# Kernel tuning notes

Measured on AMD Instinct MI355X. Metric: run time of the kernel, lower is better.

Reference implementation:

```python
import jax, jax.numpy as jnp
import numpy as np

D_MODEL = 1024
N_HEADS = 16
SEQ = 512  # == max_seq_len; rel-pos bias requires n_token == max_seq_len


def setup_inputs() -> dict:
    key = jax.random.key(0)
    ks = jax.random.split(key, 12)
    B = 16
    x = jax.random.normal(ks[0], (B, SEQ, D_MODEL), dtype=jnp.float32)
    c = jax.random.normal(ks[1], (B, SEQ, 8), dtype=jnp.float32)  # unused by forward
    s = 1.0 / np.sqrt(D_MODEL)
    Wq = jax.random.normal(ks[2], (D_MODEL, D_MODEL), dtype=jnp.float32) * s
    bq = jnp.zeros((D_MODEL,), dtype=jnp.float32)
    Wk = jax.random.normal(ks[3], (D_MODEL, D_MODEL), dtype=jnp.float32) * s
    bk = jnp.zeros((D_MODEL,), dtype=jnp.float32)
    Wv = jax.random.normal(ks[4], (D_MODEL, D_MODEL), dtype=jnp.float32) * s
    bv = jnp.zeros((D_MODEL,), dtype=jnp.float32)
    Wo = jax.random.normal(ks[5], (D_MODEL, D_MODEL), dtype=jnp.float32) * s
    bo = jnp.zeros((D_MODEL,), dtype=jnp.float32)
    # trunc_normal_(std=0.02) approximated by normal*0.02 (values stay small)
    rel_table = jax.random.normal(ks[6], (2 * SEQ - 1, N_HEADS), dtype=jnp.float32) * 0.02
    return {"x": x, "c": c, "Wq": Wq, "bq": bq, "Wk": Wk, "bk": bk,
            "Wv": Wv, "bv": bv, "Wo": Wo, "bo": bo, "rel_table": rel_table}


def reference(x, c, Wq, bq, Wk, bk, Wv, bv, Wo, bo, rel_table):
    # x: [B, S, D]; c is unused in the original forward
    B, S, D = x.shape
    H = N_HEADS
    dk = D // H
    scale = 1.0 / np.sqrt(dk)

    q = (x @ Wq + bq).reshape(B, S, H, dk)
    k = (x @ Wk + bk).reshape(B, S, H, dk)
    v = (x @ Wv + bv).reshape(B, S, H, dk)

    # scores: [B, H, S, S]
    scores = jnp.einsum('bihd,bjhd->bhij', q, k) * scale

    # relative position bias: index[i,j] = i + (S-1-j), values in [0, 2S-2]
    rel_index = jnp.arange(S)[:, None] + jnp.arange(S - 1, -1, -1)[None, :]  # [S,S]
    bias = rel_table[rel_index]            # [S, S, H]
    scores = scores + jnp.transpose(bias, (2, 0, 1))[None]  # [1,H,S,S]

    # causal_mask=False: original adds False * -1e9 == 0, so no mask term
    probs = jax.nn.softmax(scores, axis=-1)

    out = jnp.einsum('bhij,bjhd->bihd', probs, v).reshape(B, S, D)
    return out @ Wo + bo
```

## Files before the change

kernel.cpp:

```cpp
#include <hip/hip_runtime.h>
#include <hip/hip_bf16.h>
#include <stdint.h>

#define D_MODEL 1024
#define NH 16
#define SEQ 512
#define DK 64
#define BATCH 16
#define M_TOT (BATCH*SEQ)

typedef unsigned short u16;
typedef unsigned int u32;
typedef __attribute__((ext_vector_type(8))) __bf16 bf16x8;
typedef __attribute__((ext_vector_type(4))) u16 ushort4v;
typedef __attribute__((ext_vector_type(4))) float f32x4;

static __device__ __forceinline__ u16 f2bf(float f) {
    union { float f; u32 i; } c; c.f = f;
    return (u16)((c.i + 0x8000u) >> 16);
}
static __device__ __forceinline__ void async_copy16(const void* g, void* l) {
    __builtin_amdgcn_global_load_lds(
        (const __attribute__((address_space(1))) u32*)g,
        (__attribute__((address_space(3))) u32*)l, 16, 0, 0);
}

__global__ __launch_bounds__(256) void convert_f32_bf16(const float* __restrict__ in,
                                                        u16* __restrict__ out) {
    const int i = (blockIdx.x * 256 + threadIdx.x) * 4;
    float4 v = *(const float4*)&in[i];
    ushort4v o;
    o[0] = f2bf(v.x); o[1] = f2bf(v.y); o[2] = f2bf(v.z); o[3] = f2bf(v.w);
    *(ushort4v*)&out[i] = o;
}

__global__ __launch_bounds__(256) void transpose_w3(const float* __restrict__ W0,
                                                    const float* __restrict__ W1,
                                                    const float* __restrict__ W2,
                                                    u16* __restrict__ Wt) {
    __shared__ u16 tile[64][65];
    const int z = blockIdx.z;
    const float* W = (z == 0) ? W0 : (z == 1) ? W1 : W2;
    const int n0 = blockIdx.x * 64, k0 = blockIdx.y * 64;
    const int t = threadIdx.x;
    #pragma unroll
    for (int p = 0; p < 16; ++p) {
        int idx = p * 256 + t;
        int r = idx >> 6, c = idx & 63;
        tile[r][c] = f2bf(W[(size_t)(k0 + r) * D_MODEL + (n0 + c)]);
    }
    __syncthreads();
    #pragma unroll
    for (int p = 0; p < 16; ++p) {
        int idx = p * 256 + t;
        int r = idx >> 6, c = idx & 63;
        Wt[((size_t)z * D_MODEL + n0 + r) * D_MODEL + (k0 + c)] = tile[c][r];
    }
}

__global__ __launch_bounds__(256) void gemm_bt(const u16* __restrict__ A,
                                               const u16* __restrict__ Bt,
                                               const float* __restrict__ b0,
                                               const float* __restrict__ b1,
                                               const float* __restrict__ b2,
                                               void* __restrict__ o0,
                                               void* __restrict__ o1,
                                               void* __restrict__ o2,
                                               int qkv) {
    __shared__ __attribute__((aligned(16))) u16 smem[16896];
    u16* Asm = smem;
    u16* Bsm = smem + 8192;
    const int t = threadIdx.x;
    const int m0 = blockIdx.y * 128, n0 = blockIdx.x * 128;
    const int lane = t & 63, w = t >> 6;
    const int lm = lane & 15, quad = lane >> 4;
    const int wm = w >> 1, wn = w & 1;

    f32x4 acc[4][4];
    #pragma unroll
    for (int i = 0; i < 4; ++i)
        #pragma unroll
        for (int j = 0; j < 4; ++j) acc[i][j] = (f32x4){0.f, 0.f, 0.f, 0.f};

    for (int kt = 0; kt < D_MODEL / 64; ++kt) {
        const int k0 = kt * 64;
        __syncthreads();
        #pragma unroll
        for (int i = 0; i < 4; ++i) {
            int chunk = i * 256 + t;
            int row = chunk >> 3, c = chunk & 7;
            int cs = c ^ (row & 7);
            async_copy16(A + (size_t)(m0 + row) * D_MODEL + k0 + cs * 8, &Asm[chunk * 8]);
        }
        #pragma unroll
        for (int i = 0; i < 4; ++i) {
            int chunk = i * 256 + t;
            int row = chunk >> 3, c = chunk & 7;
            int cs = c ^ (row & 7);
            async_copy16(Bt + (size_t)(n0 + row) * D_MODEL + k0 + cs * 8, &Bsm[chunk * 8]);
        }
        __syncthreads();
        #pragma unroll
        for (int ks = 0; ks < 64; ks += 32) {
            const int cbase = ks >> 3;
            bf16x8 af[4], bfv[4];
            #pragma unroll
            for (int im = 0; im < 4; ++im) {
                const int row = wm * 64 + im * 16 + lm;
                const int c = (cbase + quad) ^ (row & 7);
                af[im] = *(const bf16x8*)&Asm[row * 64 + c * 8];
            }
            #pragma unroll
            for (int in = 0; in < 4; ++in) {
                const int row = wn * 64 + in * 16 + lm;
                const int c = (cbase + quad) ^ (row & 7);
                bfv[in] = *(const bf16x8*)&Bsm[row * 64 + c * 8];
            }
            #pragma unroll
            for (int im = 0; im < 4; ++im)
                #pragma unroll
                for (int in = 0; in < 4; ++in)
                    acc[im][in] = __builtin_amdgcn_mfma_f32_16x16x32_bf16(
                        af[im], bfv[in], acc[im][in], 0, 0, 0);
        }
    }

    __syncthreads();
    if (qkv) {
        const int sel = n0 >> 10;
        if (sel == 2) {
            #pragma unroll
            for (int in = 0; in < 4; ++in) {
                const int nn = (n0 & 1023) + wn * 64 + in * 16 + lm;
                const float bv = b2[nn];
                const int h = nn >> 6, d = nn & 63;
                #pragma unroll
                for (int im = 0; im < 4; ++im) {
                    const int mb = m0 + wm * 64 + im * 16 + quad * 4;
                    const int b = mb >> 9, s = mb & 511;
                    ushort4v pk;
                    #pragma unroll
                    for (int r = 0; r < 4; ++r) pk[r] = f2bf(acc[im][in][r] + bv);
                    *(ushort4v*)&((u16*)o2)[((size_t)(b * NH + h) * DK + d) * SEQ + s] = pk;
                }
            }
        } else {
            u16* dst = sel ? (u16*)o1 : (u16*)o0;
            const float* bb = sel ? b1 : b0;
            u16 (*Cs)[132] = (u16(*)[132])smem;
            #pragma unroll
            for (int in = 0; in < 4; ++in) {
                const int nl = wn * 64 + in * 16 + lm;
                const float bv = bb[(n0 & 1023) + nl];
                #pragma unroll
                for (int im = 0; im < 4; ++im)
                    #pragma unroll
                    for (int r = 0; r < 4; ++r)
                        Cs[wm * 64 + im * 16 + quad * 4 + r][nl] =
                            f2bf(acc[im][in][r] + bv);
            }
            __syncthreads();
            const int rr = t >> 1, hh = t & 1;
            const int m = m0 + rr;
            const int b = m >> 9, s = m & 511;
            const int h = ((n0 & 1023) >> 6) + hh;
            u16* dp = &dst[((size_t)(b * NH + h) * SEQ + s) * DK];
            #pragma unroll
            for (int c = 0; c < 8; ++c)
                *(uint4*)&dp[c * 8] = *(const uint4*)&Cs[rr][hh * 64 + c * 8];
        }
    } else {
        float (*Cs)[132] = (float(*)[132])smem;
        #pragma unroll
        for (int ph = 0; ph < 2; ++ph) {
            if (wm == ph) {
                #pragma unroll
                for (int in = 0; in < 4; ++in) {
                    const int nl = wn * 64 + in * 16 + lm;
                    const float bv = b0[n0 + nl];
                    #pragma unroll
                    for (int im = 0; im < 4; ++im)
                        #pragma unroll
                        for (int r = 0; r < 4; ++r)
                            Cs[im * 16 + quad * 4 + r][nl] = acc[im][in][r] + bv;
                }
            }
            __syncthreads();
            const int rr = t >> 2, qq = t & 3;
            float* dp = &((float*)o0)[(size_t)(m0 + ph * 64 + rr) * D_MODEL + n0 + qq * 32];
            #pragma unroll
            for (int c = 0; c < 8; ++c)
                *(uint4*)&dp[c * 4] = *(const uint4*)&Cs[rr][qq * 32 + c * 4];
            __syncthreads();
        }
    }
}

__global__ __launch_bounds__(256) void attn_flash(const u16* __restrict__ qg,
                                                  const u16* __restrict__ kg,
                                                  const u16* __restrict__ vTg,
                                                  const float* __restrict__ rel,
                                                  u16* __restrict__ aout) {
    __shared__ __attribute__((aligned(16))) u16 qt[64][72];
    __shared__ __attribute__((aligned(16))) u16 kt[64][72];
    __shared__ __attribute__((aligned(16))) u16 vt[64][72];
    __shared__ __attribute__((aligned(16))) u16 Pl[4][16][72];
    __shared__ float biasb[576];

    const int t = threadIdx.x;
    const int lane = t & 63, w = t >> 6;
    const int lm = lane & 15, quad = lane >> 4;
    const int F = blockIdx.x;
    const int xcd = F & 7, qti = (F >> 3) & 7, grp = F >> 6;
    const int p = grp * 8 + xcd;
    const int h = p & 15, b = p >> 4;
    const int q0 = qti * 64;
    const size_t bh = (size_t)(b * NH + h);
    const u16* qb = qg + bh * SEQ * DK;
    const u16* kb = kg + bh * SEQ * DK;
    const u16* vb = vTg + bh * DK * SEQ;

    const int srow = t >> 3, scol = (t & 7) * 8;

    #pragma unroll
    for (int i = 0; i < 2; ++i)
        *(uint4*)&qt[i * 32 + srow][scol] = *(const uint4*)&qb[(q0 + i * 32 + srow) * DK + scol];
    for (int u = t; u < 575; u += 256) biasb[u] = rel[(q0 + u) * NH + h];

    uint4 kr[2], vr[2];
    kr[0] = *(const uint4*)&kb[srow * DK + scol];
    kr[1] = *(const uint4*)&kb[(32 + srow) * DK + scol];
    vr[0] = *(const uint4*)&vb[srow * SEQ + scol];
    vr[1] = *(const uint4*)&vb[(32 + srow) * SEQ + scol];

    float lsum[4] = {0.f, 0.f, 0.f, 0.f};
    f32x4 o[4];
    #pragma unroll
    for (int sd = 0; sd < 4; ++sd) o[sd] = (f32x4){0.f, 0.f, 0.f, 0.f};

    const float scale = 0.125f;

    for (int jt = 0; jt < 8; ++jt) {
        __syncthreads();
        *(uint4*)&kt[srow][scol] = kr[0];
        *(uint4*)&kt[32 + srow][scol] = kr[1];
        *(uint4*)&vt[srow][scol] = vr[0];
        *(uint4*)&vt[32 + srow][scol] = vr[1];
        __syncthreads();
        if (jt < 7) {
            const int j1 = (jt + 1) * 64;
            kr[0] = *(const uint4*)&kb[(j1 + srow) * DK + scol];
            kr[1] = *(const uint4*)&kb[(j1 + 32 + srow) * DK + scol];
            vr[0] = *(const uint4*)&vb[srow * SEQ + j1 + scol];
            vr[1] = *(const uint4*)&vb[(32 + srow) * SEQ + j1 + scol];
        }
        const int j0 = jt * 64;

        bf16x8 aq0 = *(const bf16x8*)&qt[w * 16 + lm][quad * 8];
        bf16x8 aq1 = *(const bf16x8*)&qt[w * 16 + lm][32 + quad * 8];
        #pragma unroll
        for (int js = 0; js < 4; ++js) {
            bf16x8 bk0 = *(const bf16x8*)&kt[js * 16 + lm][quad * 8];
            bf16x8 bk1 = *(const bf16x8*)&kt[js * 16 + lm][32 + quad * 8];
            f32x4 c = (f32x4){0.f, 0.f, 0.f, 0.f};
            c = __builtin_amdgcn_mfma_f32_16x16x32_bf16(aq0, bk0, c, 0, 0, 0);
            c = __builtin_amdgcn_mfma_f32_16x16x32_bf16(aq1, bk1, c, 0, 0, 0);
            const int jg = j0 + js * 16 + lm;
            #pragma unroll
            for (int r = 0; r < 4; ++r) {
                const int rl = w * 16 + quad * 4 + r;
                float e = __expf(c[r] * scale + biasb[rl + 511 - jg]);
                lsum[r] += e;
                Pl[w][quad * 4 + r][js * 16 + lm] = f2bf(e);
            }
        }

        bf16x8 ap0 = *(const bf16x8*)&Pl[w][lm][quad * 8];
        bf16x8 ap1 = *(const bf16x8*)&Pl[w][lm][32 + quad * 8];
        #pragma unroll
        for (int sd = 0; sd < 4; ++sd) {
            bf16x8 bv0 = *(const bf16x8*)&vt[sd * 16 + lm][quad * 8];
            bf16x8 bv1 = *(const bf16x8*)&vt[sd * 16 + lm][32 + quad * 8];
            o[sd] = __builtin_amdgcn_mfma_f32_16x16x32_bf16(ap0, bv0, o[sd], 0, 0, 0);
            o[sd] = __builtin_amdgcn_mfma_f32_16x16x32_bf16(ap1, bv1, o[sd], 0, 0, 0);
        }
    }

    #pragma unroll
    for (int r = 0; r < 4; ++r) {
        float s = lsum[r];
        s += __shfl_xor(s, 1, 64);
        s += __shfl_xor(s, 2, 64);
        s += __shfl_xor(s, 4, 64);
        s += __shfl_xor(s, 8, 64);
        const float rinv = 1.0f / s;
        const int srow2 = q0 + w * 16 + quad * 4 + r;
        #pragma unroll
        for (int sd = 0; sd < 4; ++sd)
            aout[(size_t)(b * SEQ + srow2) * D_MODEL + h * DK + sd * 16 + lm] =
                f2bf(o[sd][r] * rinv);
    }
}

extern "C" void kernel_launch(void* const* d_in, const int* in_sizes, int n_in,
                              void* d_out, int out_size, void* d_ws, size_t ws_size,
                              hipStream_t stream) {
    const float* x   = (const float*)d_in[0];
    const float* Wq  = (const float*)d_in[2];
    const float* bq  = (const float*)d_in[3];
    const float* Wk  = (const float*)d_in[4];
    const float* bk  = (const float*)d_in[5];
    const float* Wv  = (const float*)d_in[6];
    const float* bv  = (const float*)d_in[7];
    const float* Wo  = (const float*)d_in[8];
    const float* bo  = (const float*)d_in[9];
    const float* rel = (const float*)d_in[10];
    float* out = (float*)d_out;

    u16* ws = (u16*)d_ws;
    const size_t WSZ = (size_t)D_MODEL * D_MODEL;
    const size_t TSZ = (size_t)M_TOT * D_MODEL;
    u16* Wt3 = ws;
    u16* xbf = Wt3 + 3 * WSZ;
    u16* qws = xbf + TSZ;
    u16* kws = qws + TSZ;
    u16* vws = kws + TSZ;
    u16* aws = xbf;

    dim3 tb(256);
    convert_f32_bf16<<<dim3(M_TOT * D_MODEL / 1024), tb, 0, stream>>>(x, xbf);
    transpose_w3<<<dim3(16, 16, 3), tb, 0, stream>>>(Wq, Wk, Wv, Wt3);
    gemm_bt<<<dim3(24, 64), tb, 0, stream>>>(xbf, Wt3, bq, bk, bv, qws, kws, vws, 1);
    attn_flash<<<dim3(2048), tb, 0, stream>>>(qws, kws, vws, rel, aws);
    transpose_w3<<<dim3(16, 16, 1), tb, 0, stream>>>(Wo, Wo, Wo, Wt3);
    gemm_bt<<<dim3(8, 64), tb, 0, stream>>>(aws, Wt3, bo, nullptr, nullptr,
                                            (void*)out, nullptr, nullptr, 0);
}
```

Baseline: 301.2 us.

## Double-buffer K/V tiles with async LDS copies and coalesce attention output via head-major layout

Measured after the change: 264.5 us. 12.2% less time.

```diff
diff --git a/kernel.cpp b/kernel.cpp
--- a/kernel.cpp
+++ b/kernel.cpp
@@ -90,7 +90,15 @@
             int chunk = i * 256 + t;
             int row = chunk >> 3, c = chunk & 7;
             int cs = c ^ (row & 7);
-            async_copy16(A + (size_t)(m0 + row) * D_MODEL + k0 + cs * 8, &Asm[chunk * 8]);
+            const u16* src;
+            if (qkv) {
+                src = A + (size_t)(m0 + row) * D_MODEL + k0 + cs * 8;
+            } else {
+                const int m = m0 + row, g = kt * 8 + cs;
+                const int b = m >> 9, s = m & 511, h = g >> 3;
+                src = A + ((size_t)(b * NH + h) * SEQ + s) * DK + (g & 7) * 8;
+            }
+            async_copy16(src, &Asm[chunk * 8]);
         }
         #pragma unroll
         for (int i = 0; i < 4; ++i) {
@@ -201,9 +209,9 @@
                                                   const u16* __restrict__ vTg,
                                                   const float* __restrict__ rel,
                                                   u16* __restrict__ aout) {
-    __shared__ __attribute__((aligned(16))) u16 qt[64][72];
-    __shared__ __attribute__((aligned(16))) u16 kt[64][72];
-    __shared__ __attribute__((aligned(16))) u16 vt[64][72];
+    __shared__ __attribute__((aligned(16))) u16 qt[64 * 64];
+    __shared__ __attribute__((aligned(16))) u16 kt[2][64 * 64];
+    __shared__ __attribute__((aligned(16))) u16 vt[2][64 * 64];
     __shared__ __attribute__((aligned(16))) u16 Pl[4][16][72];
     __shared__ float biasb[576];
 
@@ -220,18 +228,21 @@
     const u16* kb = kg + bh * SEQ * DK;
     const u16* vb = vTg + bh * DK * SEQ;
 
-    const int srow = t >> 3, scol = (t & 7) * 8;
-
-    #pragma unroll
-    for (int i = 0; i < 2; ++i)
-        *(uint4*)&qt[i * 32 + srow][scol] = *(const uint4*)&qb[(q0 + i * 32 + srow) * DK + scol];
+    #pragma unroll
+    for (int i = 0; i < 2; ++i) {
+        const int chunk = i * 256 + t, row = chunk >> 3, c = chunk & 7;
+        const int cs = c ^ (row & 7);
+        *(uint4*)&qt[chunk * 8] = *(const uint4*)&qb[(q0 + row) * DK + cs * 8];
+    }
     for (int u = t; u < 575; u += 256) biasb[u] = rel[(q0 + u) * NH + h];
 
-    uint4 kr[2], vr[2];
-    kr[0] = *(const uint4*)&kb[srow * DK + scol];
-    kr[1] = *(const uint4*)&kb[(32 + srow) * DK + scol];
-    vr[0] = *(const uint4*)&vb[srow * SEQ + scol];
-    vr[1] = *(const uint4*)&vb[(32 + srow) * SEQ + scol];
+    #pragma unroll
+    for (int i = 0; i < 2; ++i) {
+        const int chunk = i * 256 + t, row = chunk >> 3, c = chunk & 7;
+        const int cs = c ^ (row & 7);
+        async_copy16(kb + row * DK + cs * 8, &kt[0][chunk * 8]);
+        async_copy16(vb + row * SEQ + cs * 8, &vt[0][chunk * 8]);
+    }
 
     float lsum[4] = {0.f, 0.f, 0.f, 0.f};
     f32x4 o[4];
@@ -242,26 +253,27 @@
 
     for (int jt = 0; jt < 8; ++jt) {
         __syncthreads();
-        *(uint4*)&kt[srow][scol] = kr[0];
-        *(uint4*)&kt[32 + srow][scol] = kr[1];
-        *(uint4*)&vt[srow][scol] = vr[0];
-        *(uint4*)&vt[32 + srow][scol] = vr[1];
-        __syncthreads();
+        const int cur = jt & 1, nxt = cur ^ 1;
         if (jt < 7) {
             const int j1 = (jt + 1) * 64;
-            kr[0] = *(const uint4*)&kb[(j1 + srow) * DK + scol];
-            kr[1] = *(const uint4*)&kb[(j1 + 32 + srow) * DK + scol];
-            vr[0] = *(const uint4*)&vb[srow * SEQ + j1 + scol];
-            vr[1] = *(const uint4*)&vb[(32 + srow) * SEQ + j1 + scol];
+            #pragma unroll
+            for (int i = 0; i < 2; ++i) {
+                const int chunk = i * 256 + t, row = chunk >> 3, c = chunk & 7;
+                const int cs = c ^ (row & 7);
+                async_copy16(kb + (j1 + row) * DK + cs * 8, &kt[nxt][chunk * 8]);
+                async_copy16(vb + row * SEQ + j1 + cs * 8, &vt[nxt][chunk * 8]);
+            }
         }
         const int j0 = jt * 64;
 
-        bf16x8 aq0 = *(const bf16x8*)&qt[w * 16 + lm][quad * 8];
-        bf16x8 aq1 = *(const bf16x8*)&qt[w * 16 + lm][32 + quad * 8];
+        const int ra = w * 16 + lm;
+        bf16x8 aq0 = *(const bf16x8*)&qt[ra * 64 + ((quad) ^ (ra & 7)) * 8];
+        bf16x8 aq1 = *(const bf16x8*)&qt[ra * 64 + ((4 + quad) ^ (ra & 7)) * 8];
         #pragma unroll
         for (int js = 0; js < 4; ++js) {
-            bf16x8 bk0 = *(const bf16x8*)&kt[js * 16 + lm][quad * 8];
-            bf16x8 bk1 = *(const bf16x8*)&kt[js * 16 + lm][32 + quad * 8];
+            const int rb = js * 16 + lm;
+            bf16x8 bk0 = *(const bf16x8*)&kt[cur][rb * 64 + ((quad) ^ (rb & 7)) * 8];
+            bf16x8 bk1 = *(const bf16x8*)&kt[cur][rb * 64 + ((4 + quad) ^ (rb & 7)) * 8];
             f32x4 c = (f32x4){0.f, 0.f, 0.f, 0.f};
             c = __builtin_amdgcn_mfma_f32_16x16x32_bf16(aq0, bk0, c, 0, 0, 0);
             c = __builtin_amdgcn_mfma_f32_16x16x32_bf16(aq1, bk1, c, 0, 0, 0);
@@ -279,8 +291,9 @@
         bf16x8 ap1 = *(const bf16x8*)&Pl[w][lm][32 + quad * 8];
         #pragma unroll
         for (int sd = 0; sd < 4; ++sd) {
-            bf16x8 bv0 = *(const bf16x8*)&vt[sd * 16 + lm][quad * 8];
-            bf16x8 bv1 = *(const bf16x8*)&vt[sd * 16 + lm][32 + quad * 8];
+            const int rv = sd * 16 + lm;
+            bf16x8 bv0 = *(const bf16x8*)&vt[cur][rv * 64 + ((quad) ^ (rv & 7)) * 8];
+            bf16x8 bv1 = *(const bf16x8*)&vt[cur][rv * 64 + ((4 + quad) ^ (rv & 7)) * 8];
             o[sd] = __builtin_amdgcn_mfma_f32_16x16x32_bf16(ap0, bv0, o[sd], 0, 0, 0);
             o[sd] = __builtin_amdgcn_mfma_f32_16x16x32_bf16(ap1, bv1, o[sd], 0, 0, 0);
         }
@@ -294,12 +307,14 @@
         s += __shfl_xor(s, 4, 64);
         s += __shfl_xor(s, 8, 64);
         const float rinv = 1.0f / s;
-        const int srow2 = q0 + w * 16 + quad * 4 + r;
         #pragma unroll
         for (int sd = 0; sd < 4; ++sd)
-            aout[(size_t)(b * SEQ + srow2) * D_MODEL + h * DK + sd * 16 + lm] =
-                f2bf(o[sd][r] * rinv);
-    }
+            Pl[w][quad * 4 + r][sd * 16 + lm] = f2bf(o[sd][r] * rinv);
+    }
+    const int rowl = lane >> 2, ch = lane & 3;
+    u16* dp = aout + bh * SEQ * DK + (size_t)(q0 + w * 16 + rowl) * DK + ch * 16;
+    *(uint4*)&dp[0] = *(const uint4*)&Pl[w][rowl][ch * 16];
+    *(uint4*)&dp[8] = *(const uint4*)&Pl[w][rowl][ch * 16 + 8];
 }
 
 extern "C" void kernel_launch(void* const* d_in, const int* in_sizes, int n_in,
```
